# Optimization experiments

Hardware: AMD Instinct MI355X
Metric: run time of the kernel (lower is better)

The kernel has to match this reference:

```python
import jax, jax.numpy as jnp
import numpy as np

H = 4; HID = 128; NEG = 0.2
N_GEN, N_BUS, N_RES = 50000, 80000, 10000
N = N_GEN + N_BUS + N_RES
E_PROD, E_SERV, E_TRAN, E_BACK = 100000, 100000, 150000, 50000


def _lrelu(x):
    return jnp.where(x >= 0, x, NEG * x)


def _heat_layer(x, src, dst, node_type, edge_type, edge_attr, hW, hb, ete, eae, attw, linw):
    # HeteroLinear: x @ W[node_type] + b[node_type] (compute for all 3 types, select)
    xt = jnp.einsum('nd,tdo->nto', x, hW)                                  # [N,3,HID]
    x = jnp.take_along_axis(xt, node_type[:, None, None], axis=1)[:, 0, :] + hb[node_type]
    etee = _lrelu(ete[edge_type])                                          # [E,16]
    eaee = _lrelu(edge_attr @ eae)                                         # [E,16]
    x_i = x[dst]                                                           # target nodes
    x_j = x[src]                                                           # source nodes
    a = _lrelu(jnp.concatenate([x_i, x_j, etee, eaee], axis=-1) @ attw)    # [E,H]
    # softmax over incoming edges of each target node (PyG softmax: eps=1e-16)
    m = jax.ops.segment_max(a, dst, num_segments=N)                        # [N,H]
    a = jnp.exp(a - m[dst])
    denom = jax.ops.segment_sum(a, dst, num_segments=N)
    alpha = a / (denom[dst] + 1e-16)                                       # [E,H]
    msg = jnp.concatenate([x_j, eaee], axis=-1) @ linw                     # [E,HID]
    # concat=False -> mean over heads of alpha[:,h,None]*msg; fold the head
    # mean into alpha to avoid the [E,H,HID] intermediate (identical math).
    return jax.ops.segment_sum(msg * alpha.mean(axis=-1, keepdims=True), dst, num_segments=N)


def _forward(x_gen, x_bus, x_res, ea_prod, ea_served, ea_trans, ea_backed,
             pW_gen, pb_gen, pW_bus, pb_bus, pW_res, pb_res,
             hW1, hb1, ete1, eae1, attw1, linw1,
             hW2, hb2, ete2, eae2, attw2, linw2,
             hW3, hb3, ete3, eae3, attw3, linw3,
             ei_prod, ei_served, ei_trans, ei_backed):
    x = jnp.concatenate([x_gen @ pW_gen + pb_gen,
                         x_bus @ pW_bus + pb_bus,
                         x_res @ pW_res + pb_res], axis=0)                  # [N,HID]
    node_type = jnp.concatenate([jnp.full((N_GEN,), 0, jnp.int32),
                                 jnp.full((N_BUS,), 1, jnp.int32),
                                 jnp.full((N_RES,), 2, jnp.int32)])
    ei = jnp.concatenate([ei_prod, ei_served, ei_trans, ei_backed], axis=1)
    src, dst = ei[0], ei[1]
    edge_attr = jnp.concatenate([ea_prod, ea_served, ea_trans, ea_backed], axis=0)
    edge_type = jnp.concatenate([jnp.full((E_PROD,), 0, jnp.int32),
                                 jnp.full((E_SERV,), 1, jnp.int32),
                                 jnp.full((E_TRAN,), 2, jnp.int32),
                                 jnp.full((E_BACK,), 3, jnp.int32)])
    x1 = jax.nn.relu(_heat_layer(x, src, dst, node_type, edge_type, edge_attr,
                                 hW1, hb1, ete1, eae1, attw1, linw1))
    x2 = jax.nn.relu(_heat_layer(x1, src, dst, node_type, edge_type, edge_attr,
                                 hW2, hb2, ete2, eae2, attw2, linw2)) + x1
    x3 = jax.nn.relu(_heat_layer(x2, src, dst, node_type, edge_type, edge_attr,
                                 hW3, hb3, ete3, eae3, attw3, linw3)) + x2
    return x3  # dropout is identity in eval mode


def setup_inputs() -> dict:
    key = jax.random.key(0)
    ks = iter(jax.random.split(key, 64))

    def nrm(shape, s=0.05):
        return jax.random.normal(next(ks), shape, jnp.float32) * s

    def eidx(n_e, slo, shi, dlo, dhi):
        s = jax.random.randint(next(ks), (n_e,), slo, shi, dtype=jnp.int32)
        d = jax.random.randint(next(ks), (n_e,), dlo, dhi, dtype=jnp.int32)
        return jnp.stack([s, d], axis=0)

    inp = {
        'x_gen': nrm((N_GEN, 39), 1.0),
        'x_bus': nrm((N_BUS, 16), 1.0),
        'x_res': nrm((N_RES, 16), 1.0),
        'ei_prod': eidx(E_PROD, 0, N_GEN, N_GEN, N_GEN + N_BUS),
        'ei_served': eidx(E_SERV, N_GEN, N_GEN + N_BUS, 0, N_GEN),
        'ei_trans': eidx(E_TRAN, N_GEN, N_GEN + N_BUS, N_GEN, N_GEN + N_BUS),
        'ei_backed': eidx(E_BACK, N_GEN + N_BUS, N, 0, N_GEN),
        'ea_prod': nrm((E_PROD, 2), 1.0),
        'ea_served': nrm((E_SERV, 2), 1.0),
        'ea_trans': nrm((E_TRAN, 2), 1.0),
        'ea_backed': nrm((E_BACK, 2), 1.0),
        'pW_gen': nrm((39, HID)), 'pb_gen': nrm((HID,)),
        'pW_bus': nrm((16, HID)), 'pb_bus': nrm((HID,)),
        'pW_res': nrm((16, HID)), 'pb_res': nrm((HID,)),
    }
    for l in (1, 2, 3):
        inp[f'hW{l}'] = nrm((3, HID, HID))
        inp[f'hb{l}'] = nrm((3, HID))
        inp[f'ete{l}'] = nrm((4, 16))
        inp[f'eae{l}'] = nrm((2, 16))
        inp[f'attw{l}'] = nrm((2 * HID + 16 + 16, H))
        inp[f'linw{l}'] = nrm((HID + 16, HID))
    return inp


def reference(x_gen, x_bus, x_res, ei_prod, ei_served, ei_trans, ei_backed,
              ea_prod, ea_served, ea_trans, ea_backed,
              pW_gen, pb_gen, pW_bus, pb_bus, pW_res, pb_res,
              hW1, hb1, ete1, eae1, attw1, linw1,
              hW2, hb2, ete2, eae2, attw2, linw2,
              hW3, hb3, ete3, eae3, attw3, linw3):
    return _forward(x_gen, x_bus, x_res, ea_prod, ea_served, ea_trans, ea_backed,
                    pW_gen, pb_gen, pW_bus, pb_bus, pW_res, pb_res,
                    hW1, hb1, ete1, eae1, attw1, linw1,
                    hW2, hb2, ete2, eae2, attw2, linw2,
                    hW3, hb3, ete3, eae3, attw3, linw3,
                    ei_prod, ei_served, ei_trans, ei_backed)
```

## Files before the change

kernel.cpp:

```cpp
#include <hip/hip_runtime.h>
#include <hip/hip_bf16.h>

#define NGEN 50000
#define NBUS 80000
#define NRES 10000
#define NTOT 140000
#define EPROD 100000
#define ESERV 100000
#define ETRAN 150000
#define EBACK 50000
#define ETOT  400000
#define HID 128
#define NEGS 0.2f

#define NB_SCAN 547
#define EB 1563
#define WB 35000
#define NW16 8750
#define PGRID 768
#define AGGW 160
#define LINP 172
#define HETP 140

typedef __attribute__((ext_vector_type(8))) short bf16x8;
typedef __attribute__((ext_vector_type(8))) unsigned short u16x8;
typedef __attribute__((ext_vector_type(4))) float f32x4;

__device__ __forceinline__ float lrelu(float x) { return x >= 0.f ? x : NEGS * x; }
__device__ __forceinline__ float b2f(ushort u) { union { float f; uint i; } v; v.i = (uint)u << 16; return v.f; }
__device__ __forceinline__ ushort f2b(float f) {
  union { float f; uint i; } v; v.f = f;
  return (ushort)((v.i + 0x7FFF + ((v.i >> 16) & 1)) >> 16);
}

__global__ __launch_bounds__(256) void k_setup_edges(
    const int* __restrict__ eip, const int* __restrict__ eis,
    const int* __restrict__ eit, const int* __restrict__ eib,
    const float* __restrict__ eap, const float* __restrict__ eas,
    const float* __restrict__ eat, const float* __restrict__ eab,
    int* __restrict__ esrc, int* __restrict__ edst, float* __restrict__ ea_all,
    int* __restrict__ cnt)
{
  int e = blockIdx.x * 256 + threadIdx.x;
  if (e >= ETOT) return;
  int s, d; float a0, a1;
  if (e < EPROD) { s = eip[e]; d = eip[EPROD + e]; a0 = eap[2*e]; a1 = eap[2*e+1]; }
  else if (e < EPROD+ESERV) { int i = e - EPROD; s = eis[i]; d = eis[ESERV + i]; a0 = eas[2*i]; a1 = eas[2*i+1]; }
  else if (e < EPROD+ESERV+ETRAN) { int i = e - EPROD - ESERV; s = eit[i]; d = eit[ETRAN + i]; a0 = eat[2*i]; a1 = eat[2*i+1]; }
  else { int i = e - EPROD - ESERV - ETRAN; s = eib[i]; d = eib[EBACK + i]; a0 = eab[2*i]; a1 = eab[2*i+1]; }
  esrc[e] = s; edst[e] = d; ea_all[2*e] = a0; ea_all[2*e+1] = a1;
  atomicAdd(&cnt[d], 1);
}

__global__ __launch_bounds__(256) void k_scan1(const int* __restrict__ cnt,
                                               int* __restrict__ rp, int* __restrict__ bsum)
{
  int t = threadIdx.x, i = blockIdx.x * 256 + t;
  int v = (i < NTOT) ? cnt[i] : 0;
  __shared__ int buf[256];
  buf[t] = v; __syncthreads();
  for (int off = 1; off < 256; off <<= 1) {
    int x = (t >= off) ? buf[t - off] : 0;
    __syncthreads(); buf[t] += x; __syncthreads();
  }
  if (i < NTOT) rp[i] = buf[t] - v;
  if (t == 255) bsum[blockIdx.x] = buf[255];
}

__global__ __launch_bounds__(1024) void k_scan2(int* __restrict__ bsum, int nb)
{
  int t = threadIdx.x;
  __shared__ int buf[1024];
  int v = (t < nb) ? bsum[t] : 0;
  buf[t] = v; __syncthreads();
  for (int off = 1; off < 1024; off <<= 1) {
    int x = (t >= off) ? buf[t - off] : 0;
    __syncthreads(); buf[t] += x; __syncthreads();
  }
  if (t < nb) bsum[t] = buf[t] - v;
}

__global__ __launch_bounds__(256) void k_scan3(int* __restrict__ rp, const int* __restrict__ bsum)
{
  int i = blockIdx.x * 256 + threadIdx.x;
  if (i < NTOT) rp[i] += bsum[blockIdx.x];
  if (i == 0) rp[NTOT] = ETOT;
}

__global__ __launch_bounds__(256) void k_scatter(const int* __restrict__ esrc,
    const int* __restrict__ edst, const int* __restrict__ rp,
    int* __restrict__ fill, int2* __restrict__ plist)
{
  int e = blockIdx.x * 256 + threadIdx.x;
  if (e >= ETOT) return;
  int d = edst[e];
  int pos = rp[d] + atomicAdd(&fill[d], 1);
  plist[pos] = make_int2(esrc[e], e);
}

__global__ __launch_bounds__(256) void k_convW(
    const float* __restrict__ pg, const float* __restrict__ pb, const float* __restrict__ pr,
    const float* __restrict__ h1, const float* __restrict__ l1,
    const float* __restrict__ h2, const float* __restrict__ l2,
    const float* __restrict__ h3, const float* __restrict__ l3,
    ushort* __restrict__ dst)
{
  int idx = blockIdx.x * 256 + threadIdx.x;
  if (idx >= 233472) return;
  const float* src; int K, KP, base;
  if (idx < 24576) {
    int s = idx >> 13;
    src = (s == 0) ? pg : (s == 1) ? pb : pr;
    K = (s == 0) ? 39 : 16; KP = 64; base = s * 8192;
  } else {
    int r = idx - 24576, l = r / 69632, q = r % 69632;
    const float* h = (l == 0) ? h1 : (l == 1) ? h2 : h3;
    const float* lw = (l == 0) ? l1 : (l == 1) ? l2 : l3;
    if (q < 49152) { int t = q >> 14; src = h + t * 16384; K = 128; KP = 128; base = 24576 + l * 69632 + t * 16384; }
    else { src = lw; K = 144; KP = 160; base = 24576 + l * 69632 + 49152; }
  }
  int li = idx - base, c = li / KP, k = li % KP;
  dst[idx] = (k < K) ? f2b(src[k * 128 + c]) : (ushort)0;
}

struct Seg {
  const void* A; const ushort* Wt; const float* bias;
  int lda, K, M, nb, rbase;
};

__global__ __launch_bounds__(256) void k_mgemm3(Seg s0, Seg s1, Seg s2, int KP, ushort* __restrict__ Cb)
{
  __shared__ ushort As[128][72];
  __shared__ ushort Bs[128][72];
  int bid = blockIdx.x;
  Seg sg = s0;
  if (bid >= s0.nb + s1.nb) { sg = s2; bid -= s0.nb + s1.nb; }
  else if (bid >= s0.nb) { sg = s1; bid -= s0.nb; }

  const int tid = threadIdx.x;
  const int lr = tid & 15, hi = (tid & 63) >> 4;
  const int w = tid >> 6;
  const int wrow = (w >> 1) * 64, wcol = (w & 1) * 64;
  const int brow = bid * 128;

  f32x4 acc[4][4];
#pragma unroll
  for (int m = 0; m < 4; ++m)
#pragma unroll
    for (int n = 0; n < 4; ++n) acc[m][n] = (f32x4){0.f, 0.f, 0.f, 0.f};

  for (int k0 = 0; k0 < KP; k0 += 64) {
#pragma unroll
    for (int p = 0; p < 8; ++p) {
      int li = tid + 256 * p;
      int row = li >> 4, c4 = (li & 15) * 4;
      int gr = brow + row, gk = k0 + c4;
      ushort4 u = make_ushort4(0, 0, 0, 0);
      if (gr < sg.M) {
        const float* A = (const float*)sg.A;
        const float* ar = A + (size_t)gr * sg.lda;
        if (gk + 0 < sg.K) u.x = f2b(ar[gk + 0]);
        if (gk + 1 < sg.K) u.y = f2b(ar[gk + 1]);
        if (gk + 2 < sg.K) u.z = f2b(ar[gk + 2]);
        if (gk + 3 < sg.K) u.w = f2b(ar[gk + 3]);
      }
      *(ushort4*)&As[row][c4] = u;
    }
#pragma unroll
    for (int p = 0; p < 8; ++p) {
      int li = tid + 256 * p;
      int row = li >> 4, c4 = (li & 15) * 4;
      *(ushort4*)&Bs[row][c4] = *(const ushort4*)&sg.Wt[(size_t)row * KP + k0 + c4];
    }
    __syncthreads();
#pragma unroll
    for (int kk = 0; kk < 64; kk += 32) {
      bf16x8 af[4], bfv[4];
#pragma unroll
      for (int m = 0; m < 4; ++m) af[m] = *(const bf16x8*)&As[wrow + m * 16 + lr][kk + hi * 8];
#pragma unroll
      for (int n = 0; n < 4; ++n) bfv[n] = *(const bf16x8*)&Bs[wcol + n * 16 + lr][kk + hi * 8];
#pragma unroll
      for (int m = 0; m < 4; ++m)
#pragma unroll
        for (int n = 0; n < 4; ++n)
          acc[m][n] = __builtin_amdgcn_mfma_f32_16x16x32_bf16(af[m], bfv[n], acc[m][n], 0, 0, 0);
    }
    __syncthreads();
  }

#pragma unroll
  for (int m = 0; m < 4; ++m) {
#pragma unroll
    for (int j = 0; j < 4; ++j) {
      int gr = brow + wrow + m * 16 + hi * 4 + j;
      if (gr >= sg.M) continue;
#pragma unroll
      for (int n = 0; n < 4; ++n) {
        int col = wcol + n * 16 + lr;
        float v = acc[m][n][j] + sg.bias[col];
        Cb[(size_t)(sg.rbase + gr) * 128 + col] = f2b(v);
      }
    }
  }
}

__global__ __launch_bounds__(256) void k_wgemm_het(
    const ushort* __restrict__ A,
    const ushort* __restrict__ WtH,
    const float* __restrict__ hb,
    const float* __restrict__ attw,
    ushort* __restrict__ xh,
    float* __restrict__ sd, float* __restrict__ ss)
{
  __shared__ ushort Ws[128 * HETP];
  __shared__ float atw[1152];
  const int tid = threadIdx.x;
  const int bid = blockIdx.x;
  int seg, lb, nb, ntile, segbase, segrows;
  if (bid < 274)      { seg = 0; lb = bid;       nb = 274; ntile = 782;  segbase = 0;           segrows = NGEN; }
  else if (bid < 712) { seg = 1; lb = bid - 274; nb = 438; ntile = 1250; segbase = NGEN;        segrows = NBUS; }
  else                { seg = 2; lb = bid - 712; nb = 56;  ntile = 157;  segbase = NGEN + NBUS; segrows = NRES; }

  const int w = tid >> 6;
  const int lane = tid & 63;
  const int lr = lane & 15, hi = lane >> 4;

  int rl = lb * 64 + w * 16;
  int valid = rl < segrows;
  int r0 = segbase + (valid ? rl : 0);
  const ushort* Ap = A + (size_t)(r0 + lr) * 128 + hi * 8;
  bf16x8 a0 = *(const bf16x8*)(Ap);
  bf16x8 a1 = *(const bf16x8*)(Ap + 32);
  bf16x8 a2 = *(const bf16x8*)(Ap + 64);
  bf16x8 a3 = *(const bf16x8*)(Ap + 96);

  {
    const ushort* src = WtH + seg * 16384 + tid * 64;
    ushort* dstl = Ws + (tid >> 1) * HETP + (tid & 1) * 64;
#pragma unroll
    for (int j = 0; j < 8; ++j)
      *(u16x8*)&dstl[j * 8] = *(const u16x8*)&src[j * 8];
    for (int i = tid; i < 1152; i += 256) atw[i] = attw[i];
  }
  __syncthreads();

  const float* bias = hb + seg * 128;

  for (int t = lb; t < ntile; t += nb) {
    const int curvalid = valid, currow = r0;
    bf16x8 c0 = a0, c1 = a1, c2 = a2, c3 = a3;

    int tn = t + nb;
    if (tn < ntile) {
      rl = tn * 64 + w * 16;
      valid = rl < segrows;
      r0 = segbase + (valid ? rl : 0);
      const ushort* An = A + (size_t)(r0 + lr) * 128 + hi * 8;
      a0 = *(const bf16x8*)(An);
      a1 = *(const bf16x8*)(An + 32);
      a2 = *(const bf16x8*)(An + 64);
      a3 = *(const bf16x8*)(An + 96);
    }
    if (!curvalid) continue;

    f32x4 acc[8];
#pragma unroll
    for (int n = 0; n < 8; ++n) acc[n] = (f32x4){0.f, 0.f, 0.f, 0.f};
    const ushort* wb0 = Ws + lr * HETP + hi * 8;
#pragma unroll
    for (int n = 0; n < 8; ++n) {
      const ushort* wn = wb0 + n * 16 * HETP;
      acc[n] = __builtin_amdgcn_mfma_f32_16x16x32_bf16(*(const bf16x8*)(wn),      c0, acc[n], 0, 0, 0);
      acc[n] = __builtin_amdgcn_mfma_f32_16x16x32_bf16(*(const bf16x8*)(wn + 32), c1, acc[n], 0, 0, 0);
      acc[n] = __builtin_amdgcn_mfma_f32_16x16x32_bf16(*(const bf16x8*)(wn + 64), c2, acc[n], 0, 0, 0);
      acc[n] = __builtin_amdgcn_mfma_f32_16x16x32_bf16(*(const bf16x8*)(wn + 96), c3, acc[n], 0, 0, 0);
    }

    const int row = currow + lr;
    float pd0 = 0.f, pd1 = 0.f, pd2 = 0.f, pd3 = 0.f;
    float ps0 = 0.f, ps1 = 0.f, ps2 = 0.f, ps3 = 0.f;
#pragma unroll
    for (int n = 0; n < 8; ++n) {
      int c0i = n * 16 + hi * 4;
      float4 bv = *(const float4*)&bias[c0i];
      f32x4 v = acc[n];
      v[0] += bv.x; v[1] += bv.y; v[2] += bv.z; v[3] += bv.w;
      *(ushort4*)&xh[(size_t)row * 128 + c0i] = make_ushort4(f2b(v[0]), f2b(v[1]), f2b(v[2]), f2b(v[3]));
#pragma unroll
      for (int j = 0; j < 4; ++j) {
        float4 wd = *(const float4*)&atw[(c0i + j) * 4];
        float4 ws = *(const float4*)&atw[(128 + c0i + j) * 4];
        pd0 += v[j] * wd.x; pd1 += v[j] * wd.y; pd2 += v[j] * wd.z; pd3 += v[j] * wd.w;
        ps0 += v[j] * ws.x; ps1 += v[j] * ws.y; ps2 += v[j] * ws.z; ps3 += v[j] * ws.w;
      }
    }
    pd0 += __shfl_xor(pd0, 16); pd0 += __shfl_xor(pd0, 32);
    pd1 += __shfl_xor(pd1, 16); pd1 += __shfl_xor(pd1, 32);
    pd2 += __shfl_xor(pd2, 16); pd2 += __shfl_xor(pd2, 32);
    pd3 += __shfl_xor(pd3, 16); pd3 += __shfl_xor(pd3, 32);
    ps0 += __shfl_xor(ps0, 16); ps0 += __shfl_xor(ps0, 32);
    ps1 += __shfl_xor(ps1, 16); ps1 += __shfl_xor(ps1, 32);
    ps2 += __shfl_xor(ps2, 16); ps2 += __shfl_xor(ps2, 32);
    ps3 += __shfl_xor(ps3, 16); ps3 += __shfl_xor(ps3, 32);
    if (hi == 0) {
      float4 o = {pd0, pd1, pd2, pd3};
      *(float4*)&sd[row * 4] = o;
    } else if (hi == 1) {
      float4 o = {ps0, ps1, ps2, ps3};
      *(float4*)&ss[row * 4] = o;
    }
  }
}

template<int HASRES, int LAST>
__global__ __launch_bounds__(256) void k_wgemm_lin(
    const ushort* __restrict__ A,
    const ushort* __restrict__ Wt,
    const ushort* residb,
    float* __restrict__ Cf,
    ushort* Cb)
{
  __shared__ ushort Ws[128 * LINP];
  const int tid = threadIdx.x;
  const int lane = tid & 63;
  const int lr = lane & 15, hi = lane >> 4;
  const int w = tid >> 6;

  int gw = blockIdx.x * 4 + w;
  const ushort* Ar0 = A + (size_t)(gw * 16 + lr) * AGGW + hi * 8;
  bf16x8 a0 = *(const bf16x8*)(Ar0);
  bf16x8 a1 = *(const bf16x8*)(Ar0 + 32);
  bf16x8 a2 = *(const bf16x8*)(Ar0 + 64);
  bf16x8 a3 = *(const bf16x8*)(Ar0 + 96);
  bf16x8 a4 = *(const bf16x8*)(Ar0 + 128);

  {
    const ushort* src = Wt + tid * 80;
    ushort* dstl = Ws + (tid >> 1) * LINP + (tid & 1) * 80;
#pragma unroll
    for (int j = 0; j < 10; ++j)
      *(u16x8*)&dstl[j * 8] = *(const u16x8*)&src[j * 8];
  }
  __syncthreads();

  for (; gw < NW16; gw += PGRID * 4) {
    const int gcur = gw;
    bf16x8 c0 = a0, c1 = a1, c2 = a2, c3 = a3, c4 = a4;
    int gn = gw + PGRID * 4;
    if (gn < NW16) {
      const ushort* An = A + (size_t)(gn * 16 + lr) * AGGW + hi * 8;
      a0 = *(const bf16x8*)(An);
      a1 = *(const bf16x8*)(An + 32);
      a2 = *(const bf16x8*)(An + 64);
      a3 = *(const bf16x8*)(An + 96);
      a4 = *(const bf16x8*)(An + 128);
    }

    f32x4 acc[8];
#pragma unroll
    for (int n = 0; n < 8; ++n) acc[n] = (f32x4){0.f, 0.f, 0.f, 0.f};
    const ushort* wb0 = Ws + lr * LINP + hi * 8;
#pragma unroll
    for (int n = 0; n < 8; ++n) {
      const ushort* wn = wb0 + n * 16 * LINP;
      acc[n] = __builtin_amdgcn_mfma_f32_16x16x32_bf16(*(const bf16x8*)(wn),       c0, acc[n], 0, 0, 0);
      acc[n] = __builtin_amdgcn_mfma_f32_16x16x32_bf16(*(const bf16x8*)(wn + 32),  c1, acc[n], 0, 0, 0);
      acc[n] = __builtin_amdgcn_mfma_f32_16x16x32_bf16(*(const bf16x8*)(wn + 64),  c2, acc[n], 0, 0, 0);
      acc[n] = __builtin_amdgcn_mfma_f32_16x16x32_bf16(*(const bf16x8*)(wn + 96),  c3, acc[n], 0, 0, 0);
      acc[n] = __builtin_amdgcn_mfma_f32_16x16x32_bf16(*(const bf16x8*)(wn + 128), c4, acc[n], 0, 0, 0);
    }

    const int row = gcur * 16 + lr;
#pragma unroll
    for (int n = 0; n < 8; ++n) {
      int c0i = n * 16 + hi * 4;
      f32x4 v = acc[n];
      v[0] = fmaxf(v[0], 0.f); v[1] = fmaxf(v[1], 0.f);
      v[2] = fmaxf(v[2], 0.f); v[3] = fmaxf(v[3], 0.f);
      if (HASRES) {
        ushort4 r = *(const ushort4*)&residb[(size_t)row * 128 + c0i];
        v[0] += b2f(r.x); v[1] += b2f(r.y); v[2] += b2f(r.z); v[3] += b2f(r.w);
      }
      if (LAST) {
        *(f32x4*)&Cf[(size_t)row * 128 + c0i] = v;
      } else {
        *(ushort4*)&Cb[(size_t)row * 128 + c0i] =
            make_ushort4(f2b(v[0]), f2b(v[1]), f2b(v[2]), f2b(v[3]));
      }
    }
  }
}

__global__ __launch_bounds__(256) void k_edge(
    const int* __restrict__ esrc, const int* __restrict__ edst,
    const float* __restrict__ ea_all, const float* __restrict__ eae,
    const float* __restrict__ attw, const float* __restrict__ ete,
    const float* __restrict__ sd, const float* __restrict__ ss,
    ushort* __restrict__ eaeeB, float* __restrict__ a4buf)
{
  __shared__ float tc[4][4];
  if (threadIdx.x < 16) {
    int tt = threadIdx.x >> 2, h = threadIdx.x & 3;
    float s = 0.f;
    for (int j = 0; j < 16; ++j) s += lrelu(ete[tt * 16 + j]) * attw[(256 + j) * 4 + h];
    tc[tt][h] = s;
  }
  __syncthreads();

  int e = blockIdx.x * 256 + threadIdx.x;
  if (e >= ETOT) return;
  int t = (e < EPROD) ? 0 : (e < EPROD + ESERV) ? 1 : (e < EPROD + ESERV + ETRAN) ? 2 : 3;
  float a0 = ea_all[2 * e], a1 = ea_all[2 * e + 1];
  int s = esrc[e], d = edst[e];
  float4 sdv = *(const float4*)&sd[d * 4];
  float4 ssv = *(const float4*)&ss[s * 4];
  float acc[4] = {sdv.x + ssv.x + tc[t][0], sdv.y + ssv.y + tc[t][1],
                  sdv.z + ssv.z + tc[t][2], sdv.w + ssv.w + tc[t][3]};
  ushort us[16];
#pragma unroll
  for (int j = 0; j < 16; ++j) {
    float v = lrelu(a0 * eae[j] + a1 * eae[16 + j]);
    us[j] = f2b(v);
    float4 aw = *(const float4*)&attw[(272 + j) * 4];
    acc[0] += v * aw.x; acc[1] += v * aw.y; acc[2] += v * aw.z; acc[3] += v * aw.w;
  }
  *(ushort4*)&eaeeB[(size_t)e * 16 + 0]  = make_ushort4(us[0], us[1], us[2], us[3]);
  *(ushort4*)&eaeeB[(size_t)e * 16 + 4]  = make_ushort4(us[4], us[5], us[6], us[7]);
  *(ushort4*)&eaeeB[(size_t)e * 16 + 8]  = make_ushort4(us[8], us[9], us[10], us[11]);
  *(ushort4*)&eaeeB[(size_t)e * 16 + 12] = make_ushort4(us[12], us[13], us[14], us[15]);
  float4 out = {lrelu(acc[0]), lrelu(acc[1]), lrelu(acc[2]), lrelu(acc[3])};
  *(float4*)&a4buf[e * 4] = out;
}

__global__ __launch_bounds__(256) void k_softmax(
    const int* __restrict__ rp, const int2* __restrict__ plist,
    const float* __restrict__ a4buf, float* __restrict__ ab)
{
  int n = blockIdx.x * 256 + threadIdx.x;
  if (n >= NTOT) return;
  int beg = rp[n], end = rp[n + 1];
  if (beg == end) return;
  float m0 = -INFINITY, m1 = -INFINITY, m2 = -INFINITY, m3 = -INFINITY;
  for (int i = beg; i < end; ++i) {
    int e = plist[i].y;
    float4 av = *(const float4*)&a4buf[(size_t)e * 4];
    m0 = fmaxf(m0, av.x); m1 = fmaxf(m1, av.y); m2 = fmaxf(m2, av.z); m3 = fmaxf(m3, av.w);
  }
  float d0 = 0.f, d1 = 0.f, d2 = 0.f, d3 = 0.f;
  for (int i = beg; i < end; ++i) {
    int e = plist[i].y;
    float4 av = *(const float4*)&a4buf[(size_t)e * 4];
    d0 += __expf(av.x - m0); d1 += __expf(av.y - m1);
    d2 += __expf(av.z - m2); d3 += __expf(av.w - m3);
  }
  d0 = 1.f / (d0 + 1e-16f); d1 = 1.f / (d1 + 1e-16f);
  d2 = 1.f / (d2 + 1e-16f); d3 = 1.f / (d3 + 1e-16f);
  for (int i = beg; i < end; ++i) {
    int e = plist[i].y;
    float4 av = *(const float4*)&a4buf[(size_t)e * 4];
    ab[i] = 0.25f * (__expf(av.x - m0) * d0 + __expf(av.y - m1) * d1 +
                     __expf(av.z - m2) * d2 + __expf(av.w - m3) * d3);
  }
}

__global__ __launch_bounds__(256) void k_gather(
    const int* __restrict__ rp, const int2* __restrict__ plist,
    const float* __restrict__ ab, const ushort* __restrict__ eaeeB,
    const ushort* __restrict__ xh, ushort* __restrict__ agg)
{
  int wid = (blockIdx.x * 256 + threadIdx.x) >> 6;
  int lane = threadIdx.x & 63;
  if (wid >= NTOT) return;
  int beg = rp[wid], end = rp[wid + 1];
  int deg = end - beg;
  const int l2 = lane & 31;
  const int half = lane >> 5;
  size_t rb = (size_t)wid * AGGW;

  if (deg == 0) {
    *(ushort2*)&agg[rb + lane * 2] = make_ushort2(0, 0);
    if (lane < 16) *(ushort2*)&agg[rb + 128 + lane * 2] = make_ushort2(0, 0);
    return;
  }

  f32x4 axv = (f32x4){0.f, 0.f, 0.f, 0.f};
  float ae0 = 0.f, ae1 = 0.f;

  if (deg <= 64) {
    int sj = 0, ej = 0; float wj = 0.f;
    if (lane < deg) {
      int2 pe = plist[beg + lane];
      sj = pe.x; ej = pe.y;
      wj = ab[beg + lane];
    }
    for (int j0 = 0; j0 < deg; j0 += 2) {
      int j = j0 + half;
      bool jv = j < deg;
      int jj = jv ? j : 0;
      float wab = jv ? __shfl(wj, jj) : 0.f;
      int s = __shfl(sj, jj);
      int e = __shfl(ej, jj);
      ushort4 xv = *(const ushort4*)&xh[(size_t)s * 128 + l2 * 4];
      axv[0] += wab * b2f(xv.x); axv[1] += wab * b2f(xv.y);
      axv[2] += wab * b2f(xv.z); axv[3] += wab * b2f(xv.w);
      if (l2 < 8) {
        ushort2 q = *(const ushort2*)&eaeeB[(size_t)e * 16 + l2 * 2];
        ae0 += wab * b2f(q.x); ae1 += wab * b2f(q.y);
      }
    }
  } else {
    for (int i = beg; i < end; i += 2) {
      int idx = i + half;
      bool valid = idx < end;
      int idc = valid ? idx : beg;
      int2 pe = plist[idc];
      float w = valid ? ab[idc] : 0.f;
      ushort4 xv = *(const ushort4*)&xh[(size_t)pe.x * 128 + l2 * 4];
      axv[0] += w * b2f(xv.x); axv[1] += w * b2f(xv.y);
      axv[2] += w * b2f(xv.z); axv[3] += w * b2f(xv.w);
      if (l2 < 8) {
        ushort2 q = *(const ushort2*)&eaeeB[(size_t)pe.y * 16 + l2 * 2];
        ae0 += w * b2f(q.x); ae1 += w * b2f(q.y);
      }
    }
  }
#pragma unroll
  for (int j = 0; j < 4; ++j) axv[j] += __shfl_xor(axv[j], 32);
  ae0 += __shfl_xor(ae0, 32); ae1 += __shfl_xor(ae1, 32);

  if (half == 0) {
    *(ushort4*)&agg[rb + l2 * 4] =
        make_ushort4(f2b(axv[0]), f2b(axv[1]), f2b(axv[2]), f2b(axv[3]));
  } else {
    if (l2 < 8) *(ushort2*)&agg[rb + 128 + l2 * 2] = make_ushort2(f2b(ae0), f2b(ae1));
    else if (l2 < 16) *(ushort2*)&agg[rb + 144 + (l2 - 8) * 2] = make_ushort2(0, 0);
  }
}

extern "C" void kernel_launch(void* const* d_in, const int* in_sizes, int n_in,
                              void* d_out, int out_size, void* d_ws, size_t ws_size,
                              hipStream_t stream)
{
  const float* x_gen = (const float*)d_in[0];
  const float* x_bus = (const float*)d_in[1];
  const float* x_res = (const float*)d_in[2];
  const int* eip = (const int*)d_in[3];
  const int* eis = (const int*)d_in[4];
  const int* eit = (const int*)d_in[5];
  const int* eib = (const int*)d_in[6];
  const float* eap = (const float*)d_in[7];
  const float* eas = (const float*)d_in[8];
  const float* eat = (const float*)d_in[9];
  const float* eab = (const float*)d_in[10];
  const float* pW_gen = (const float*)d_in[11];
  const float* pb_gen = (const float*)d_in[12];
  const float* pW_bus = (const float*)d_in[13];
  const float* pb_bus = (const float*)d_in[14];
  const float* pW_res = (const float*)d_in[15];
  const float* pb_res = (const float*)d_in[16];

  float* out = (float*)d_out;

  char* p = (char*)d_ws;
  auto alloc = [&](size_t bytes) -> void* {
    void* r = (void*)p;
    p += (bytes + 255) & ~(size_t)255;
    return r;
  };
  int* esrc    = (int*)alloc((size_t)ETOT * 4);
  int* edst    = (int*)alloc((size_t)ETOT * 4);
  float* ea_all = (float*)alloc((size_t)ETOT * 2 * 4);
  int* cnt     = (int*)alloc((size_t)NTOT * 4);
  int* fill    = (int*)alloc((size_t)NTOT * 4);
  int* rp      = (int*)alloc((size_t)(NTOT + 1) * 4);
  int* bsum    = (int*)alloc(1024 * 4);
  int2* plist  = (int2*)alloc((size_t)ETOT * 8);
  float* ab    = (float*)alloc((size_t)ETOT * 4);
  ushort* Wt   = (ushort*)alloc((size_t)233472 * 2);
  ushort* x_bf = (ushort*)alloc((size_t)NTOT * HID * 2);
  ushort* xh_bf = (ushort*)alloc((size_t)NTOT * HID * 2);
  float* sd    = (float*)alloc((size_t)NTOT * 4 * 4);
  float* ss    = (float*)alloc((size_t)NTOT * 4 * 4);
  ushort* eaeeB = (ushort*)alloc((size_t)ETOT * 16 * 2);
  float* a4buf = (float*)alloc((size_t)ETOT * 4 * 4);
  ushort* agg  = (ushort*)alloc((size_t)NTOT * AGGW * 2);

  hipMemsetAsync(cnt, 0, (size_t)NTOT * 4, stream);
  hipMemsetAsync(fill, 0, (size_t)NTOT * 4, stream);
  k_setup_edges<<<EB, 256, 0, stream>>>(eip, eis, eit, eib, eap, eas, eat, eab, esrc, edst, ea_all, cnt);
  k_scan1<<<NB_SCAN, 256, 0, stream>>>(cnt, rp, bsum);
  k_scan2<<<1, 1024, 0, stream>>>(bsum, NB_SCAN);
  k_scan3<<<NB_SCAN, 256, 0, stream>>>(rp, bsum);
  k_scatter<<<EB, 256, 0, stream>>>(esrc, edst, rp, fill, plist);

  k_convW<<<912, 256, 0, stream>>>(pW_gen, pW_bus, pW_res,
      (const float*)d_in[17], (const float*)d_in[22],
      (const float*)d_in[23], (const float*)d_in[28],
      (const float*)d_in[29], (const float*)d_in[34], Wt);

  const int NB0 = (NGEN + 127) / 128, NB1 = (NBUS + 127) / 128, NB2 = (NRES + 127) / 128;
  const int NBT = NB0 + NB1 + NB2;

  {
    Seg s0{x_gen, Wt + 0,     pb_gen, 39, 39, NGEN, NB0, 0};
    Seg s1{x_bus, Wt + 8192,  pb_bus, 16, 16, NBUS, NB1, NGEN};
    Seg s2{x_res, Wt + 16384, pb_res, 16, 16, NRES, NB2, NGEN + NBUS};
    k_mgemm3<<<NBT, 256, 0, stream>>>(s0, s1, s2, 64, x_bf);
  }

  for (int l = 0; l < 3; ++l) {
    const float* hb   = (const float*)d_in[18 + l * 6];
    const float* ete  = (const float*)d_in[19 + l * 6];
    const float* eae  = (const float*)d_in[20 + l * 6];
    const float* attw = (const float*)d_in[21 + l * 6];
    const ushort* WtH = Wt + 24576 + l * 69632;
    const ushort* WtL = Wt + 24576 + l * 69632 + 49152;

    k_wgemm_het<<<PGRID, 256, 0, stream>>>(x_bf, WtH, hb, attw, xh_bf, sd, ss);

    k_edge<<<EB, 256, 0, stream>>>(esrc, edst, ea_all, eae, attw, ete, sd, ss, eaeeB, a4buf);
    k_softmax<<<NB_SCAN, 256, 0, stream>>>(rp, plist, a4buf, ab);
    k_gather<<<WB, 256, 0, stream>>>(rp, plist, ab, eaeeB, xh_bf, agg);

    if (l == 0)      k_wgemm_lin<0,0><<<PGRID, 256, 0, stream>>>(agg, WtL, nullptr, nullptr, x_bf);
    else if (l == 1) k_wgemm_lin<1,0><<<PGRID, 256, 0, stream>>>(agg, WtL, x_bf, nullptr, x_bf);
    else             k_wgemm_lin<1,1><<<PGRID, 256, 0, stream>>>(agg, WtL, x_bf, out, nullptr);
  }
}
```

Baseline: 577.3 us.

## Store edge attention and features in CSR order to make softmax/gather reads contiguous

The scatter kernel now records each edge's CSR position. The edge kernel writes its attention logits and edge embeddings directly at that position, so softmax and gather read them sequentially rather than through an edge-id indirection. The int2 plist becomes a plain source-index array. Separately, the het GEMM drops its shared-memory copy of the attention weights and reads them from global memory instead. The edge kernel's writes become scattered in exchange for contiguous reads downstream.

```diff
diff --git a/kernel.cpp b/kernel.cpp
--- a/kernel.cpp
+++ b/kernel.cpp
@@ -89,13 +89,14 @@
 
 __global__ __launch_bounds__(256) void k_scatter(const int* __restrict__ esrc,
     const int* __restrict__ edst, const int* __restrict__ rp,
-    int* __restrict__ fill, int2* __restrict__ plist)
+    int* __restrict__ fill, int* __restrict__ srcp, int* __restrict__ epos)
 {
   int e = blockIdx.x * 256 + threadIdx.x;
   if (e >= ETOT) return;
   int d = edst[e];
   int pos = rp[d] + atomicAdd(&fill[d], 1);
-  plist[pos] = make_int2(esrc[e], e);
+  srcp[pos] = esrc[e];
+  epos[e] = pos;
 }
 
 __global__ __launch_bounds__(256) void k_convW(
@@ -214,7 +215,6 @@
     float* __restrict__ sd, float* __restrict__ ss)
 {
   __shared__ ushort Ws[128 * HETP];
-  __shared__ float atw[1152];
   const int tid = threadIdx.x;
   const int bid = blockIdx.x;
   int seg, lb, nb, ntile, segbase, segrows;
@@ -241,7 +241,6 @@
 #pragma unroll
     for (int j = 0; j < 8; ++j)
       *(u16x8*)&dstl[j * 8] = *(const u16x8*)&src[j * 8];
-    for (int i = tid; i < 1152; i += 256) atw[i] = attw[i];
   }
   __syncthreads();
 
@@ -289,8 +288,8 @@
       *(ushort4*)&xh[(size_t)row * 128 + c0i] = make_ushort4(f2b(v[0]), f2b(v[1]), f2b(v[2]), f2b(v[3]));
 #pragma unroll
       for (int j = 0; j < 4; ++j) {
-        float4 wd = *(const float4*)&atw[(c0i + j) * 4];
-        float4 ws = *(const float4*)&atw[(128 + c0i + j) * 4];
+        float4 wd = *(const float4*)&attw[(c0i + j) * 4];
+        float4 ws = *(const float4*)&attw[(128 + c0i + j) * 4];
         pd0 += v[j] * wd.x; pd1 += v[j] * wd.y; pd2 += v[j] * wd.z; pd3 += v[j] * wd.w;
         ps0 += v[j] * ws.x; ps1 += v[j] * ws.y; ps2 += v[j] * ws.z; ps3 += v[j] * ws.w;
       }
@@ -394,6 +393,7 @@
 
 __global__ __launch_bounds__(256) void k_edge(
     const int* __restrict__ esrc, const int* __restrict__ edst,
+    const int* __restrict__ epos,
     const float* __restrict__ ea_all, const float* __restrict__ eae,
     const float* __restrict__ attw, const float* __restrict__ ete,
     const float* __restrict__ sd, const float* __restrict__ ss,
@@ -413,6 +413,7 @@
   int t = (e < EPROD) ? 0 : (e < EPROD + ESERV) ? 1 : (e < EPROD + ESERV + ETRAN) ? 2 : 3;
   float a0 = ea_all[2 * e], a1 = ea_all[2 * e + 1];
   int s = esrc[e], d = edst[e];
+  int pos = epos[e];
   float4 sdv = *(const float4*)&sd[d * 4];
   float4 ssv = *(const float4*)&ss[s * 4];
   float acc[4] = {sdv.x + ssv.x + tc[t][0], sdv.y + ssv.y + tc[t][1],
@@ -425,16 +426,16 @@
     float4 aw = *(const float4*)&attw[(272 + j) * 4];
     acc[0] += v * aw.x; acc[1] += v * aw.y; acc[2] += v * aw.z; acc[3] += v * aw.w;
   }
-  *(ushort4*)&eaeeB[(size_t)e * 16 + 0]  = make_ushort4(us[0], us[1], us[2], us[3]);
-  *(ushort4*)&eaeeB[(size_t)e * 16 + 4]  = make_ushort4(us[4], us[5], us[6], us[7]);
-  *(ushort4*)&eaeeB[(size_t)e * 16 + 8]  = make_ushort4(us[8], us[9], us[10], us[11]);
-  *(ushort4*)&eaeeB[(size_t)e * 16 + 12] = make_ushort4(us[12], us[13], us[14], us[15]);
+  *(ushort4*)&eaeeB[(size_t)pos * 16 + 0]  = make_ushort4(us[0], us[1], us[2], us[3]);
+  *(ushort4*)&eaeeB[(size_t)pos * 16 + 4]  = make_ushort4(us[4], us[5], us[6], us[7]);
+  *(ushort4*)&eaeeB[(size_t)pos * 16 + 8]  = make_ushort4(us[8], us[9], us[10], us[11]);
+  *(ushort4*)&eaeeB[(size_t)pos * 16 + 12] = make_ushort4(us[12], us[13], us[14], us[15]);
   float4 out = {lrelu(acc[0]), lrelu(acc[1]), lrelu(acc[2]), lrelu(acc[3])};
-  *(float4*)&a4buf[e * 4] = out;
+  *(float4*)&a4buf[(size_t)pos * 4] = out;
 }
 
 __global__ __launch_bounds__(256) void k_softmax(
-    const int* __restrict__ rp, const int2* __restrict__ plist,
+    const int* __restrict__ rp,
     const float* __restrict__ a4buf, float* __restrict__ ab)
 {
   int n = blockIdx.x * 256 + threadIdx.x;
@@ -443,29 +444,26 @@
   if (beg == end) return;
   float m0 = -INFINITY, m1 = -INFINITY, m2 = -INFINITY, m3 = -INFINITY;
   for (int i = beg; i < end; ++i) {
-    int e = plist[i].y;
-    float4 av = *(const float4*)&a4buf[(size_t)e * 4];
+    float4 av = *(const float4*)&a4buf[(size_t)i * 4];
     m0 = fmaxf(m0, av.x); m1 = fmaxf(m1, av.y); m2 = fmaxf(m2, av.z); m3 = fmaxf(m3, av.w);
   }
   float d0 = 0.f, d1 = 0.f, d2 = 0.f, d3 = 0.f;
   for (int i = beg; i < end; ++i) {
-    int e = plist[i].y;
-    float4 av = *(const float4*)&a4buf[(size_t)e * 4];
+    float4 av = *(const float4*)&a4buf[(size_t)i * 4];
     d0 += __expf(av.x - m0); d1 += __expf(av.y - m1);
     d2 += __expf(av.z - m2); d3 += __expf(av.w - m3);
   }
   d0 = 1.f / (d0 + 1e-16f); d1 = 1.f / (d1 + 1e-16f);
   d2 = 1.f / (d2 + 1e-16f); d3 = 1.f / (d3 + 1e-16f);
   for (int i = beg; i < end; ++i) {
-    int e = plist[i].y;
-    float4 av = *(const float4*)&a4buf[(size_t)e * 4];
+    float4 av = *(const float4*)&a4buf[(size_t)i * 4];
     ab[i] = 0.25f * (__expf(av.x - m0) * d0 + __expf(av.y - m1) * d1 +
                      __expf(av.z - m2) * d2 + __expf(av.w - m3) * d3);
   }
 }
 
 __global__ __launch_bounds__(256) void k_gather(
-    const int* __restrict__ rp, const int2* __restrict__ plist,
+    const int* __restrict__ rp, const int* __restrict__ srcp,
     const float* __restrict__ ab, const ushort* __restrict__ eaeeB,
     const ushort* __restrict__ xh, ushort* __restrict__ agg)
 {
@@ -488,10 +486,9 @@
   float ae0 = 0.f, ae1 = 0.f;
 
   if (deg <= 64) {
-    int sj = 0, ej = 0; float wj = 0.f;
+    int sj = 0; float wj = 0.f;
     if (lane < deg) {
-      int2 pe = plist[beg + lane];
-      sj = pe.x; ej = pe.y;
+      sj = srcp[beg + lane];
       wj = ab[beg + lane];
     }
     for (int j0 = 0; j0 < deg; j0 += 2) {
@@ -500,12 +497,11 @@
       int jj = jv ? j : 0;
       float wab = jv ? __shfl(wj, jj) : 0.f;
       int s = __shfl(sj, jj);
-      int e = __shfl(ej, jj);
       ushort4 xv = *(const ushort4*)&xh[(size_t)s * 128 + l2 * 4];
       axv[0] += wab * b2f(xv.x); axv[1] += wab * b2f(xv.y);
       axv[2] += wab * b2f(xv.z); axv[3] += wab * b2f(xv.w);
       if (l2 < 8) {
-        ushort2 q = *(const ushort2*)&eaeeB[(size_t)e * 16 + l2 * 2];
+        ushort2 q = *(const ushort2*)&eaeeB[(size_t)(beg + jj) * 16 + l2 * 2];
         ae0 += wab * b2f(q.x); ae1 += wab * b2f(q.y);
       }
     }
@@ -514,13 +510,13 @@
       int idx = i + half;
       bool valid = idx < end;
       int idc = valid ? idx : beg;
-      int2 pe = plist[idc];
+      int s = srcp[idc];
       float w = valid ? ab[idc] : 0.f;
-      ushort4 xv = *(const ushort4*)&xh[(size_t)pe.x * 128 + l2 * 4];
+      ushort4 xv = *(const ushort4*)&xh[(size_t)s * 128 + l2 * 4];
       axv[0] += w * b2f(xv.x); axv[1] += w * b2f(xv.y);
       axv[2] += w * b2f(xv.z); axv[3] += w * b2f(xv.w);
       if (l2 < 8) {
-        ushort2 q = *(const ushort2*)&eaeeB[(size_t)pe.y * 16 + l2 * 2];
+        ushort2 q = *(const ushort2*)&eaeeB[(size_t)idc * 16 + l2 * 2];
         ae0 += w * b2f(q.x); ae1 += w * b2f(q.y);
       }
     }
@@ -575,7 +571,8 @@
   int* fill    = (int*)alloc((size_t)NTOT * 4);
   int* rp      = (int*)alloc((size_t)(NTOT + 1) * 4);
   int* bsum    = (int*)alloc(1024 * 4);
-  int2* plist  = (int2*)alloc((size_t)ETOT * 8);
+  int* srcp    = (int*)alloc((size_t)ETOT * 4);
+  int* epos    = (int*)alloc((size_t)ETOT * 4);
   float* ab    = (float*)alloc((size_t)ETOT * 4);
   ushort* Wt   = (ushort*)alloc((size_t)233472 * 2);
   ushort* x_bf = (ushort*)alloc((size_t)NTOT * HID * 2);
@@ -592,7 +589,7 @@
   k_scan1<<<NB_SCAN, 256, 0, stream>>>(cnt, rp, bsum);
   k_scan2<<<1, 1024, 0, stream>>>(bsum, NB_SCAN);
   k_scan3<<<NB_SCAN, 256, 0, stream>>>(rp, bsum);
-  k_scatter<<<EB, 256, 0, stream>>>(esrc, edst, rp, fill, plist);
+  k_scatter<<<EB, 256, 0, stream>>>(esrc, edst, rp, fill, srcp, epos);
 
   k_convW<<<912, 256, 0, stream>>>(pW_gen, pW_bus, pW_res,
       (const float*)d_in[17], (const float*)d_in[22],
@@ -619,9 +616,9 @@
 
     k_wgemm_het<<<PGRID, 256, 0, stream>>>(x_bf, WtH, hb, attw, xh_bf, sd, ss);
 
-    k_edge<<<EB, 256, 0, stream>>>(esrc, edst, ea_all, eae, attw, ete, sd, ss, eaeeB, a4buf);
-    k_softmax<<<NB_SCAN, 256, 0, stream>>>(rp, plist, a4buf, ab);
-    k_gather<<<WB, 256, 0, stream>>>(rp, plist, ab, eaeeB, xh_bf, agg);
+    k_edge<<<EB, 256, 0, stream>>>(esrc, edst, epos, ea_all, eae, attw, ete, sd, ss, eaeeB, a4buf);
+    k_softmax<<<NB_SCAN, 256, 0, stream>>>(rp, a4buf, ab);
+    k_gather<<<WB, 256, 0, stream>>>(rp, srcp, ab, eaeeB, xh_bf, agg);
 
     if (l == 0)      k_wgemm_lin<0,0><<<PGRID, 256, 0, stream>>>(agg, WtL, nullptr, nullptr, x_bf);
     else if (l == 1) k_wgemm_lin<1,0><<<PGRID, 256, 0, stream>>>(agg, WtL, x_bf, nullptr, x_bf);
```

Result: faster. 544.8 us (-5.6%).
